# Performance work log

Hardware: AMD Instinct MI355X
Metric: run time of the kernel (lower is better)

The kernel has to match this reference:

```python
import jax, jax.numpy as jnp
import numpy as np

B, N, F_IN, F_OUT = 8, 2048, 128, 128
NEG_BIG = -9e15
LEAKY_SLOPE = 0.01


def setup_inputs() -> dict:
    key = jax.random.key(0)
    k1, k2, k3, k4, k5 = jax.random.split(key, 5)
    features = jax.random.normal(k1, (B, N, F_IN), dtype=jnp.float32)
    adj_matrix = jax.random.randint(k2, (B, N, N), 0, 2, dtype=jnp.int32)
    mask = jnp.ones((B, N), dtype=jnp.float32)
    # linear: W [in,out], b [out]; attention: a [2*out] (no bias)
    W = jax.random.normal(k3, (F_IN, F_OUT), dtype=jnp.float32) / np.sqrt(F_IN)
    b = jnp.zeros((F_OUT,), dtype=jnp.float32)
    a = jax.random.normal(k4, (2 * F_OUT,), dtype=jnp.float32) / np.sqrt(2 * F_OUT)
    return {"features": features, "adj_matrix": adj_matrix, "mask": mask,
            "W": W, "b": b, "a": a}


def reference(features, adj_matrix, mask, W, b, a):
    h = jnp.einsum("bni,io->bno", features, W) + b  # [B,N,F_OUT]
    # attention(concat([h_i, h_j])) == h_i @ a_src + h_j @ a_dst
    a_src, a_dst = a[:F_OUT], a[F_OUT:]
    e = (h @ a_src)[:, :, None] + (h @ a_dst)[:, None, :]  # [B,N,N]
    e = jnp.where(e >= 0, e, LEAKY_SLOPE * e)  # leaky_relu
    scores = jnp.where(adj_matrix > 0, e, jnp.float32(NEG_BIG))
    attention = jax.nn.softmax(scores, axis=-1)
    aggregated = jnp.einsum("bnm,bmo->bno", attention, h)  # [B,N,F_OUT]
    aggregated = aggregated * mask[:, :, None]
    return aggregated
```

## Files before the change

### kernel.cpp

```cpp
#include <hip/hip_runtime.h>

#define BB 8
#define NN 2048
#define FF 128
#define RB 32
#define MT 128

typedef short bh8 __attribute__((ext_vector_type(8)));
typedef float fl4 __attribute__((ext_vector_type(4)));
typedef unsigned short u16;
typedef unsigned long long u64;

__device__ __forceinline__ u16 f2bf(float x) {
    unsigned u = __float_as_uint(x);
    return (u16)((u + 0x7FFFu + ((u >> 16) & 1u)) >> 16);
}

__global__ __launch_bounds__(256) void k_h(
    const float* __restrict__ feat, const float* __restrict__ W,
    const float* __restrict__ bias, const float* __restrict__ a,
    u16* __restrict__ htg, float* __restrict__ esrc, float* __restrict__ edst)
{
    __shared__ float fsh[8][FF];
    __shared__ float red[2][2][8];
    const int t = threadIdx.x;
    const long row0 = (long)blockIdx.x * 8;

    ((float4*)&fsh[0][0])[t] = ((const float4*)(feat + row0 * FF))[t];
    __syncthreads();

    const int o = t & 127;
    const int half = t >> 7;
    float acc[4] = {0.f, 0.f, 0.f, 0.f};
    #pragma unroll 4
    for (int k = 0; k < FF; ++k) {
        const float w = W[k * FF + o];
        #pragma unroll
        for (int r = 0; r < 4; ++r)
            acc[r] = fmaf(fsh[half * 4 + r][k], w, acc[r]);
    }
    const float bo = bias[o];
    const float as = a[o];
    const float ad = a[FF + o];
    float ps[4], pd[4];
    #pragma unroll
    for (int r = 0; r < 4; ++r) {
        acc[r] += bo;
        ps[r] = acc[r] * as;
        pd[r] = acc[r] * ad;
    }
    {
        const int bI = (int)(row0 >> 11);
        const int nloc = (int)(row0 & 2047) + half * 4;
        ushort4 hv;
        hv.x = f2bf(acc[0]); hv.y = f2bf(acc[1]);
        hv.z = f2bf(acc[2]); hv.w = f2bf(acc[3]);
        *(ushort4*)&htg[((long)bI * FF + o) * NN + nloc] = hv;
    }
    #pragma unroll
    for (int r = 0; r < 4; ++r) {
        #pragma unroll
        for (int off = 32; off > 0; off >>= 1) {
            ps[r] += __shfl_down(ps[r], off, 64);
            pd[r] += __shfl_down(pd[r], off, 64);
        }
    }
    const int wv = (t >> 6) & 1;
    if ((t & 63) == 0) {
        #pragma unroll
        for (int r = 0; r < 4; ++r) {
            red[half][wv][r]     = ps[r];
            red[half][wv][4 + r] = pd[r];
        }
    }
    __syncthreads();
    if (t < 16) {
        const int hh = t >> 3, idx = t & 7;
        const float v = red[hh][0][idx] + red[hh][1][idx];
        const long row = row0 + hh * 4 + (idx & 3);
        if (idx < 4) esrc[row] = v;
        else         edst[row] = v;
    }
}

__global__ __launch_bounds__(256) void k_pack(
    const int* __restrict__ adj, u64* __restrict__ bm)
{
    const int t = threadIdx.x;
    const int w = t >> 6, lane = t & 63;
    const long row0 = (long)blockIdx.x * 8;
    #pragma unroll 8
    for (int i = 0; i < 64; ++i) {
        const int row = 2 * w + (i >> 5);
        const int chunk = i & 31;
        const int av = adj[(row0 + row) * NN + chunk * 64 + lane];
        const u64 m64 = __ballot(av > 0);
        if (lane == 0) bm[(row0 + row) * 32 + chunk] = m64;
    }
}

__global__ __launch_bounds__(256, 2) void k_attn(
    const u64* __restrict__ bm, const float* __restrict__ mask,
    const u16* __restrict__ htg, const float* __restrict__ esrc,
    const float* __restrict__ edst, float* __restrict__ out)
{
    __shared__ float accbuf[4][RB][FF + 4];
    __shared__ float psum_sh[4][RB];

    const int t = threadIdx.x;
    const int b = blockIdx.x & 7;
    const int n0 = (blockIdx.x >> 3) * RB;
    const int w = t >> 6, lane = t & 63;
    const int lr = lane & 15, g = lane >> 4;

    float gmx = -3.4e38f;
    {
        const float4* edp = (const float4*)(edst + b * NN);
        #pragma unroll
        for (int i = 0; i < 8; ++i) {
            const float4 v = edp[lane + 64 * i];
            gmx = fmaxf(gmx, fmaxf(fmaxf(v.x, v.y), fmaxf(v.z, v.w)));
        }
        #pragma unroll
        for (int off = 32; off > 0; off >>= 1)
            gmx = fmaxf(gmx, __shfl_xor(gmx, off, 64));
    }

    const float es0 = esrc[b * NN + n0 + lr];
    const float es1 = esrc[b * NN + n0 + 16 + lr];
    const float tA = es0 + gmx; const float M0 = (tA >= 0.f) ? tA : 0.01f * tA;
    const float tB = es1 + gmx; const float M1 = (tB >= 0.f) ? tB : 0.01f * tB;

    const uint4* bmb = (const uint4*)(bm + ((long)b * NN + n0) * 32);
    const float* edb = edst + b * NN;
    const u16* hB = htg + (long)b * FF * NN;

    fl4 acc0[8], acc1[8];
    #pragma unroll
    for (int ct = 0; ct < 8; ++ct) {
        acc0[ct] = (fl4){0.f, 0.f, 0.f, 0.f};
        acc1[ct] = (fl4){0.f, 0.f, 0.f, 0.f};
    }
    float psum0 = 0.f, psum1 = 0.f;

    uint4 bmA0 = bmb[lr * 16 + w];
    uint4 bmA1 = bmb[(16 + lr) * 16 + w];

    #pragma unroll 1
    for (int it = 0; it < 4; ++it) {
        const int m0 = (w + 4 * it) * MT;
        const int base = m0 + g * 8;

        float4 ed[8];
        #pragma unroll
        for (int kc = 0; kc < 4; ++kc) {
            ed[2 * kc]     = *(const float4*)(edb + base + kc * 32);
            ed[2 * kc + 1] = *(const float4*)(edb + base + kc * 32 + 4);
        }
        bh8 bfA[8];
        #pragma unroll
        for (int ct = 0; ct < 8; ++ct)
            bfA[ct] = *(const bh8*)(hB + (long)(ct * 16 + lr) * NN + base);
        const int itn = (it + 1) & 3;
        uint4 bmB0 = bmb[lr * 16 + w + 4 * itn];
        uint4 bmB1 = bmb[(16 + lr) * 16 + w + 4 * itn];

        bh8 af0[4], af1[4];
        #pragma unroll
        for (int kc = 0; kc < 4; ++kc) {
            const unsigned w0 = (kc == 0) ? bmA0.x : (kc == 1) ? bmA0.y
                              : (kc == 2) ? bmA0.z : bmA0.w;
            const unsigned w1 = (kc == 0) ? bmA1.x : (kc == 1) ? bmA1.y
                              : (kc == 2) ? bmA1.z : bmA1.w;
            const unsigned by0 = (w0 >> (8 * g)) & 0xFFu;
            const unsigned by1 = (w1 >> (8 * g)) & 0xFFu;
            const float4 e0 = ed[2 * kc], e1 = ed[2 * kc + 1];
            const float ee[8] = {e0.x, e0.y, e0.z, e0.w, e1.x, e1.y, e1.z, e1.w};
            u16 p0[8], p1[8];
            #pragma unroll
            for (int j = 0; j < 8; ++j) {
                float x0 = es0 + ee[j]; x0 = (x0 >= 0.f) ? x0 : 0.01f * x0;
                float x1 = es1 + ee[j]; x1 = (x1 >= 0.f) ? x1 : 0.01f * x1;
                const float v0 = ((by0 >> j) & 1u) ? __expf(x0 - M0) : 0.f;
                const float v1 = ((by1 >> j) & 1u) ? __expf(x1 - M1) : 0.f;
                const u16 u0 = f2bf(v0), u1 = f2bf(v1);
                p0[j] = u0; p1[j] = u1;
                psum0 += __uint_as_float((unsigned)u0 << 16);
                psum1 += __uint_as_float((unsigned)u1 << 16);
            }
            af0[kc] = (bh8){(short)p0[0], (short)p0[1], (short)p0[2], (short)p0[3],
                            (short)p0[4], (short)p0[5], (short)p0[6], (short)p0[7]};
            af1[kc] = (bh8){(short)p1[0], (short)p1[1], (short)p1[2], (short)p1[3],
                            (short)p1[4], (short)p1[5], (short)p1[6], (short)p1[7]};
        }

        #pragma unroll
        for (int kc = 0; kc < 4; ++kc) {
            bh8 bfB[8];
            if (kc < 3) {
                #pragma unroll
                for (int ct = 0; ct < 8; ++ct)
                    bfB[ct] = *(const bh8*)(hB + (long)(ct * 16 + lr) * NN
                                            + base + (kc + 1) * 32);
            }
            #pragma unroll
            for (int ct = 0; ct < 8; ++ct) {
                acc0[ct] = __builtin_amdgcn_mfma_f32_16x16x32_bf16(af0[kc], bfA[ct], acc0[ct], 0, 0, 0);
                acc1[ct] = __builtin_amdgcn_mfma_f32_16x16x32_bf16(af1[kc], bfA[ct], acc1[ct], 0, 0, 0);
            }
            if (kc < 3) {
                #pragma unroll
                for (int ct = 0; ct < 8; ++ct) bfA[ct] = bfB[ct];
            }
        }
        bmA0 = bmB0; bmA1 = bmB1;
    }

    psum0 += __shfl_xor(psum0, 16, 64);
    psum0 += __shfl_xor(psum0, 32, 64);
    psum1 += __shfl_xor(psum1, 16, 64);
    psum1 += __shfl_xor(psum1, 32, 64);
    if (lane < 16) {
        psum_sh[w][lr] = psum0;
        psum_sh[w][16 + lr] = psum1;
    }

    #pragma unroll
    for (int ct = 0; ct < 8; ++ct)
        #pragma unroll
        for (int reg = 0; reg < 4; ++reg) {
            accbuf[w][g * 4 + reg][ct * 16 + lr]      = acc0[ct][reg];
            accbuf[w][16 + g * 4 + reg][ct * 16 + lr] = acc1[ct][reg];
        }
    __syncthreads();

    #pragma unroll
    for (int rep = 0; rep < 4; ++rep) {
        const int idx = t + 256 * rep;
        const int r = idx >> 5;
        const int c4 = (idx & 31) * 4;
        const float4 s0 = *(const float4*)&accbuf[0][r][c4];
        const float4 s1 = *(const float4*)&accbuf[1][r][c4];
        const float4 s2 = *(const float4*)&accbuf[2][r][c4];
        const float4 s3 = *(const float4*)&accbuf[3][r][c4];
        const float ps = psum_sh[0][r] + psum_sh[1][r] + psum_sh[2][r] + psum_sh[3][r];
        const float sc = mask[b * NN + n0 + r] / ps;
        float4 o;
        o.x = (s0.x + s1.x + s2.x + s3.x) * sc;
        o.y = (s0.y + s1.y + s2.y + s3.y) * sc;
        o.z = (s0.z + s1.z + s2.z + s3.z) * sc;
        o.w = (s0.w + s1.w + s2.w + s3.w) * sc;
        *(float4*)&out[((long)b * NN + n0 + r) * FF + c4] = o;
    }
}

extern "C" void kernel_launch(void* const* d_in, const int* in_sizes, int n_in,
                              void* d_out, int out_size, void* d_ws, size_t ws_size,
                              hipStream_t stream)
{
    const float* feat = (const float*)d_in[0];
    const int*   adj  = (const int*)d_in[1];
    const float* mask = (const float*)d_in[2];
    const float* W    = (const float*)d_in[3];
    const float* bias = (const float*)d_in[4];
    const float* a    = (const float*)d_in[5];
    float* out = (float*)d_out;

    u16*   htg  = (u16*)d_ws;
    float* esrc = (float*)(htg + (size_t)BB * FF * NN);
    float* edst = esrc + BB * NN;
    u64*   bmp  = (u64*)(edst + BB * NN);

    k_pack<<<BB * NN / 8, 256, 0, stream>>>(adj, bmp);
    k_h   <<<BB * NN / 8, 256, 0, stream>>>(feat, W, bias, a, htg, esrc, edst);
    k_attn<<<BB * (NN / RB), 256, 0, stream>>>(bmp, mask, htg, esrc, edst, out);
}
```

Measured before the change: 86.15 us.

## Fuse pack into projection kernel, factor exp, precompute global max, pipeline B loads

Merges the adjacency bit-packing into the projection kernel, which now also computes the per-batch max of edst with an atomicMax on order-preserving bit patterns. The projection kernel additionally stores exp(edst) and exp(0.01*edst). The attention kernel replaces its per-element exp with a multiply by per-row factors, choosing the branch by comparing against exp(-esrc). The attention loop is fully unrolled with a triple-buffered B-operand prefetch and sched barriers. The final reduction is done in registers through a smaller shared buffer, which removes one exp per score and the redundant max scan at the cost of an extra memset and more register pressure.

```diff
diff --git a/kernel.cpp b/kernel.cpp
--- a/kernel.cpp
+++ b/kernel.cpp
@@ -1,4 +1,5 @@
 #include <hip/hip_runtime.h>
+#include <hip/hip_bf16.h>
 
 #define BB 8
 #define NN 2048
@@ -10,16 +11,34 @@
 typedef float fl4 __attribute__((ext_vector_type(4)));
 typedef unsigned short u16;
 typedef unsigned long long u64;
+typedef union { bh8 v; unsigned u[4]; } bh8u;
 
 __device__ __forceinline__ u16 f2bf(float x) {
     unsigned u = __float_as_uint(x);
     return (u16)((u + 0x7FFFu + ((u >> 16) & 1u)) >> 16);
 }
 
-__global__ __launch_bounds__(256) void k_h(
-    const float* __restrict__ feat, const float* __restrict__ W,
-    const float* __restrict__ bias, const float* __restrict__ a,
-    u16* __restrict__ htg, float* __restrict__ esrc, float* __restrict__ edst)
+__device__ __forceinline__ void loadB(bh8 (&buf)[8], const u16* hB, int lr, int kbase) {
+    #pragma unroll
+    for (int ct = 0; ct < 8; ++ct)
+        buf[ct] = *(const bh8*)(hB + (ct * 16 + lr) * NN + kbase);
+}
+
+__device__ __forceinline__ void mfma16(bh8 a0, bh8 a1, const bh8 (&buf)[8],
+                                       fl4 (&c0)[8], fl4 (&c1)[8]) {
+    #pragma unroll
+    for (int ct = 0; ct < 8; ++ct) {
+        c0[ct] = __builtin_amdgcn_mfma_f32_16x16x32_bf16(a0, buf[ct], c0[ct], 0, 0, 0);
+        c1[ct] = __builtin_amdgcn_mfma_f32_16x16x32_bf16(a1, buf[ct], c1[ct], 0, 0, 0);
+    }
+}
+
+__global__ __launch_bounds__(256) void k_hp(
+    const float* __restrict__ feat, const int* __restrict__ adj,
+    const float* __restrict__ W, const float* __restrict__ bias,
+    const float* __restrict__ a, u16* __restrict__ htg,
+    float* __restrict__ esrc, float* __restrict__ eed, float* __restrict__ eed2,
+    unsigned* __restrict__ gmaxu, u64* __restrict__ bm)
 {
     __shared__ float fsh[8][FF];
     __shared__ float red[2][2][8];
@@ -78,33 +97,43 @@
         const int hh = t >> 3, idx = t & 7;
         const float v = red[hh][0][idx] + red[hh][1][idx];
         const long row = row0 + hh * 4 + (idx & 3);
-        if (idx < 4) esrc[row] = v;
-        else         edst[row] = v;
-    }
-}
-
-__global__ __launch_bounds__(256) void k_pack(
-    const int* __restrict__ adj, u64* __restrict__ bm)
-{
-    const int t = threadIdx.x;
-    const int w = t >> 6, lane = t & 63;
-    const long row0 = (long)blockIdx.x * 8;
-    #pragma unroll 8
-    for (int i = 0; i < 64; ++i) {
-        const int row = 2 * w + (i >> 5);
-        const int chunk = i & 31;
-        const int av = adj[(row0 + row) * NN + chunk * 64 + lane];
-        const u64 m64 = __ballot(av > 0);
-        if (lane == 0) bm[(row0 + row) * 32 + chunk] = m64;
+        if (idx < 4) {
+            esrc[row] = v;
+        } else {
+            eed[row]  = __expf(v);
+            eed2[row] = __expf(0.01f * v);
+        }
+        float mv = (idx >= 4) ? v : -3.4e38f;
+        #pragma unroll
+        for (int off = 8; off > 0; off >>= 1)
+            mv = fmaxf(mv, __shfl_xor(mv, off, 16));
+        if (t == 0) {
+            unsigned bu = __float_as_uint(mv);
+            bu = (bu & 0x80000000u) ? ~bu : (bu | 0x80000000u);
+            atomicMax(gmaxu + (int)(row0 >> 11), bu);
+        }
+    }
+
+    {
+        const int w2 = t >> 6, lane = t & 63;
+        #pragma unroll 8
+        for (int i = 0; i < 64; ++i) {
+            const int row = 2 * w2 + (i >> 5);
+            const int chunk = i & 31;
+            const int av = adj[(row0 + row) * NN + chunk * 64 + lane];
+            const u64 m64 = __ballot(av > 0);
+            if (lane == 0) bm[(row0 + row) * 32 + chunk] = m64;
+        }
     }
 }
 
 __global__ __launch_bounds__(256, 2) void k_attn(
     const u64* __restrict__ bm, const float* __restrict__ mask,
     const u16* __restrict__ htg, const float* __restrict__ esrc,
-    const float* __restrict__ edst, float* __restrict__ out)
+    const float* __restrict__ eed, const float* __restrict__ eed2,
+    const unsigned* __restrict__ gmaxu, float* __restrict__ out)
 {
-    __shared__ float accbuf[4][RB][FF + 4];
+    __shared__ float accbuf[2][RB][FF + 4];
     __shared__ float psum_sh[4][RB];
 
     const int t = threadIdx.x;
@@ -113,26 +142,18 @@
     const int w = t >> 6, lane = t & 63;
     const int lr = lane & 15, g = lane >> 4;
 
-    float gmx = -3.4e38f;
-    {
-        const float4* edp = (const float4*)(edst + b * NN);
-        #pragma unroll
-        for (int i = 0; i < 8; ++i) {
-            const float4 v = edp[lane + 64 * i];
-            gmx = fmaxf(gmx, fmaxf(fmaxf(v.x, v.y), fmaxf(v.z, v.w)));
-        }
-        #pragma unroll
-        for (int off = 32; off > 0; off >>= 1)
-            gmx = fmaxf(gmx, __shfl_xor(gmx, off, 64));
-    }
-
+    const unsigned gu = gmaxu[b];
+    const float gm = __uint_as_float((gu & 0x80000000u) ? (gu & 0x7FFFFFFFu) : ~gu);
     const float es0 = esrc[b * NN + n0 + lr];
     const float es1 = esrc[b * NN + n0 + 16 + lr];
-    const float tA = es0 + gmx; const float M0 = (tA >= 0.f) ? tA : 0.01f * tA;
-    const float tB = es1 + gmx; const float M1 = (tB >= 0.f) ? tB : 0.01f * tB;
+    const float m0t = es0 + gm; const float M0 = fmaxf(m0t, 0.01f * m0t);
+    const float m1t = es1 + gm; const float M1 = fmaxf(m1t, 0.01f * m1t);
+    const float A0 = __expf(es0 - M0), Bv0 = __expf(0.01f * es0 - M0), T0 = __expf(-es0);
+    const float A1 = __expf(es1 - M1), Bv1 = __expf(0.01f * es1 - M1), T1 = __expf(-es1);
 
     const uint4* bmb = (const uint4*)(bm + ((long)b * NN + n0) * 32);
-    const float* edb = edst + b * NN;
+    const float* eeb  = eed  + b * NN;
+    const float* ee2b = eed2 + b * NN;
     const u16* hB = htg + (long)b * FF * NN;
 
     fl4 acc0[8], acc1[8];
@@ -143,77 +164,73 @@
     }
     float psum0 = 0.f, psum1 = 0.f;
 
-    uint4 bmA0 = bmb[lr * 16 + w];
-    uint4 bmA1 = bmb[(16 + lr) * 16 + w];
-
-    #pragma unroll 1
+    bh8 bf0[8], bf1[8], bf2[8];
+    loadB(bf0, hB, lr, w * MT + g * 8);
+    loadB(bf1, hB, lr, w * MT + g * 8 + 32);
+    loadB(bf2, hB, lr, w * MT + g * 8 + 64);
+
+    #pragma unroll
     for (int it = 0; it < 4; ++it) {
-        const int m0 = (w + 4 * it) * MT;
-        const int base = m0 + g * 8;
-
-        float4 ed[8];
+        const int kb = (w + 4 * it) * MT + g * 8;
+        const uint4 bq0 = bmb[lr * 16 + (w + 4 * it)];
+        const uint4 bq1 = bmb[(16 + lr) * 16 + (w + 4 * it)];
+
+        bh8 af0[4], af1[4];
+        float pst0 = 0.f, pst1 = 0.f;
         #pragma unroll
         for (int kc = 0; kc < 4; ++kc) {
-            ed[2 * kc]     = *(const float4*)(edb + base + kc * 32);
-            ed[2 * kc + 1] = *(const float4*)(edb + base + kc * 32 + 4);
-        }
-        bh8 bfA[8];
-        #pragma unroll
-        for (int ct = 0; ct < 8; ++ct)
-            bfA[ct] = *(const bh8*)(hB + (long)(ct * 16 + lr) * NN + base);
-        const int itn = (it + 1) & 3;
-        uint4 bmB0 = bmb[lr * 16 + w + 4 * itn];
-        uint4 bmB1 = bmb[(16 + lr) * 16 + w + 4 * itn];
-
-        bh8 af0[4], af1[4];
+            const unsigned q0 = (kc == 0) ? bq0.x : (kc == 1) ? bq0.y : (kc == 2) ? bq0.z : bq0.w;
+            const unsigned q1 = (kc == 0) ? bq1.x : (kc == 1) ? bq1.y : (kc == 2) ? bq1.z : bq1.w;
+            const unsigned by0 = (q0 >> (8 * g)) & 0xFFu;
+            const unsigned by1 = (q1 >> (8 * g)) & 0xFFu;
+            const float4 Ea = *(const float4*)(eeb + kb + kc * 32);
+            const float4 Eb = *(const float4*)(eeb + kb + kc * 32 + 4);
+            const float4 Fa = *(const float4*)(ee2b + kb + kc * 32);
+            const float4 Fb = *(const float4*)(ee2b + kb + kc * 32 + 4);
+            const float pe[8] = {Ea.x, Ea.y, Ea.z, Ea.w, Eb.x, Eb.y, Eb.z, Eb.w};
+            const float pf[8] = {Fa.x, Fa.y, Fa.z, Fa.w, Fb.x, Fb.y, Fb.z, Fb.w};
+            bh8u pa, pb;
+            float s00 = 0.f, s01 = 0.f, s10 = 0.f, s11 = 0.f;
+            #pragma unroll
+            for (int jj = 0; jj < 4; ++jj) {
+                const int j0 = 2 * jj, j1 = 2 * jj + 1;
+                const float v00 = ((by0 >> j0) & 1u) ? ((pe[j0] >= T0) ? A0 * pe[j0] : Bv0 * pf[j0]) : 0.f;
+                const float v01 = ((by0 >> j1) & 1u) ? ((pe[j1] >= T0) ? A0 * pe[j1] : Bv0 * pf[j1]) : 0.f;
+                const float v10 = ((by1 >> j0) & 1u) ? ((pe[j0] >= T1) ? A1 * pe[j0] : Bv1 * pf[j0]) : 0.f;
+                const float v11 = ((by1 >> j1) & 1u) ? ((pe[j1] >= T1) ? A1 * pe[j1] : Bv1 * pf[j1]) : 0.f;
+                float2 c0f; c0f.x = v00; c0f.y = v01;
+                float2 c1f; c1f.x = v10; c1f.y = v11;
+                __hip_bfloat162 r0 = __float22bfloat162_rn(c0f);
+                __hip_bfloat162 r1 = __float22bfloat162_rn(c1f);
+                const unsigned u0 = *reinterpret_cast<unsigned*>(&r0);
+                const unsigned u1 = *reinterpret_cast<unsigned*>(&r1);
+                pa.u[jj] = u0;
+                pb.u[jj] = u1;
+                s00 += __uint_as_float(u0 << 16);
+                s01 += __uint_as_float(u0 & 0xFFFF0000u);
+                s10 += __uint_as_float(u1 << 16);
+                s11 += __uint_as_float(u1 & 0xFFFF0000u);
+            }
+            pst0 += s00 + s01;
+            pst1 += s10 + s11;
+            af0[kc] = pa.v;
+            af1[kc] = pb.v;
+        }
+        psum0 += pst0;
+        psum1 += pst1;
+        __builtin_amdgcn_sched_barrier(0);
+
         #pragma unroll
         for (int kc = 0; kc < 4; ++kc) {
-            const unsigned w0 = (kc == 0) ? bmA0.x : (kc == 1) ? bmA0.y
-                              : (kc == 2) ? bmA0.z : bmA0.w;
-            const unsigned w1 = (kc == 0) ? bmA1.x : (kc == 1) ? bmA1.y
-                              : (kc == 2) ? bmA1.z : bmA1.w;
-            const unsigned by0 = (w0 >> (8 * g)) & 0xFFu;
-            const unsigned by1 = (w1 >> (8 * g)) & 0xFFu;
-            const float4 e0 = ed[2 * kc], e1 = ed[2 * kc + 1];
-            const float ee[8] = {e0.x, e0.y, e0.z, e0.w, e1.x, e1.y, e1.z, e1.w};
-            u16 p0[8], p1[8];
-            #pragma unroll
-            for (int j = 0; j < 8; ++j) {
-                float x0 = es0 + ee[j]; x0 = (x0 >= 0.f) ? x0 : 0.01f * x0;
-                float x1 = es1 + ee[j]; x1 = (x1 >= 0.f) ? x1 : 0.01f * x1;
-                const float v0 = ((by0 >> j) & 1u) ? __expf(x0 - M0) : 0.f;
-                const float v1 = ((by1 >> j) & 1u) ? __expf(x1 - M1) : 0.f;
-                const u16 u0 = f2bf(v0), u1 = f2bf(v1);
-                p0[j] = u0; p1[j] = u1;
-                psum0 += __uint_as_float((unsigned)u0 << 16);
-                psum1 += __uint_as_float((unsigned)u1 << 16);
-            }
-            af0[kc] = (bh8){(short)p0[0], (short)p0[1], (short)p0[2], (short)p0[3],
-                            (short)p0[4], (short)p0[5], (short)p0[6], (short)p0[7]};
-            af1[kc] = (bh8){(short)p1[0], (short)p1[1], (short)p1[2], (short)p1[3],
-                            (short)p1[4], (short)p1[5], (short)p1[6], (short)p1[7]};
-        }
-
-        #pragma unroll
-        for (int kc = 0; kc < 4; ++kc) {
-            bh8 bfB[8];
-            if (kc < 3) {
-                #pragma unroll
-                for (int ct = 0; ct < 8; ++ct)
-                    bfB[ct] = *(const bh8*)(hB + (long)(ct * 16 + lr) * NN
-                                            + base + (kc + 1) * 32);
-            }
-            #pragma unroll
-            for (int ct = 0; ct < 8; ++ct) {
-                acc0[ct] = __builtin_amdgcn_mfma_f32_16x16x32_bf16(af0[kc], bfA[ct], acc0[ct], 0, 0, 0);
-                acc1[ct] = __builtin_amdgcn_mfma_f32_16x16x32_bf16(af1[kc], bfA[ct], acc1[ct], 0, 0, 0);
-            }
-            if (kc < 3) {
-                #pragma unroll
-                for (int ct = 0; ct < 8; ++ct) bfA[ct] = bfB[ct];
-            }
-        }
-        bmA0 = bmB0; bmA1 = bmB1;
+            const int c = it * 4 + kc;
+            bh8 (&cur)[8] = (c % 3 == 0) ? bf0 : ((c % 3 == 1) ? bf1 : bf2);
+            mfma16(af0[kc], af1[kc], cur, acc0, acc1);
+            if (c + 3 < 16) {
+                const int cn = c + 3;
+                loadB(cur, hB, lr, (w + 4 * (cn >> 2)) * MT + g * 8 + (cn & 3) * 32);
+            }
+            __builtin_amdgcn_sched_barrier(0);
+        }
     }
 
     psum0 += __shfl_xor(psum0, 16, 64);
@@ -225,32 +242,53 @@
         psum_sh[w][16 + lr] = psum1;
     }
 
-    #pragma unroll
-    for (int ct = 0; ct < 8; ++ct)
+    if (w >= 2) {
+        #pragma unroll
+        for (int ct = 0; ct < 8; ++ct)
+            #pragma unroll
+            for (int reg = 0; reg < 4; ++reg) {
+                accbuf[w - 2][g * 4 + reg][ct * 16 + lr]      = acc0[ct][reg];
+                accbuf[w - 2][16 + g * 4 + reg][ct * 16 + lr] = acc1[ct][reg];
+            }
+    }
+    __syncthreads();
+    if (w < 2) {
+        #pragma unroll
+        for (int ct = 0; ct < 8; ++ct)
+            #pragma unroll
+            for (int reg = 0; reg < 4; ++reg) {
+                acc0[ct][reg] += accbuf[w][g * 4 + reg][ct * 16 + lr];
+                acc1[ct][reg] += accbuf[w][16 + g * 4 + reg][ct * 16 + lr];
+            }
+        if (w == 1) {
+            #pragma unroll
+            for (int ct = 0; ct < 8; ++ct)
+                #pragma unroll
+                for (int reg = 0; reg < 4; ++reg) {
+                    accbuf[1][g * 4 + reg][ct * 16 + lr]      = acc0[ct][reg];
+                    accbuf[1][16 + g * 4 + reg][ct * 16 + lr] = acc1[ct][reg];
+                }
+        }
+    }
+    __syncthreads();
+    if (w == 0) {
+        const long obase = ((long)b * NN + n0) * FF;
         #pragma unroll
         for (int reg = 0; reg < 4; ++reg) {
-            accbuf[w][g * 4 + reg][ct * 16 + lr]      = acc0[ct][reg];
-            accbuf[w][16 + g * 4 + reg][ct * 16 + lr] = acc1[ct][reg];
-        }
-    __syncthreads();
-
-    #pragma unroll
-    for (int rep = 0; rep < 4; ++rep) {
-        const int idx = t + 256 * rep;
-        const int r = idx >> 5;
-        const int c4 = (idx & 31) * 4;
-        const float4 s0 = *(const float4*)&accbuf[0][r][c4];
-        const float4 s1 = *(const float4*)&accbuf[1][r][c4];
-        const float4 s2 = *(const float4*)&accbuf[2][r][c4];
-        const float4 s3 = *(const float4*)&accbuf[3][r][c4];
-        const float ps = psum_sh[0][r] + psum_sh[1][r] + psum_sh[2][r] + psum_sh[3][r];
-        const float sc = mask[b * NN + n0 + r] / ps;
-        float4 o;
-        o.x = (s0.x + s1.x + s2.x + s3.x) * sc;
-        o.y = (s0.y + s1.y + s2.y + s3.y) * sc;
-        o.z = (s0.z + s1.z + s2.z + s3.z) * sc;
-        o.w = (s0.w + s1.w + s2.w + s3.w) * sc;
-        *(float4*)&out[((long)b * NN + n0 + r) * FF + c4] = o;
+            const int r0 = g * 4 + reg;
+            const int r1 = 16 + r0;
+            const float pt0 = psum_sh[0][r0] + psum_sh[1][r0] + psum_sh[2][r0] + psum_sh[3][r0];
+            const float pt1 = psum_sh[0][r1] + psum_sh[1][r1] + psum_sh[2][r1] + psum_sh[3][r1];
+            const float sc0 = mask[b * NN + n0 + r0] / pt0;
+            const float sc1 = mask[b * NN + n0 + r1] / pt1;
+            #pragma unroll
+            for (int ct = 0; ct < 8; ++ct) {
+                out[obase + (long)r0 * FF + ct * 16 + lr] =
+                    (acc0[ct][reg] + accbuf[1][r0][ct * 16 + lr]) * sc0;
+                out[obase + (long)r1 * FF + ct * 16 + lr] =
+                    (acc1[ct][reg] + accbuf[1][r1][ct * 16 + lr]) * sc1;
+            }
+        }
     }
 }
 
@@ -266,12 +304,14 @@
     const float* a    = (const float*)d_in[5];
     float* out = (float*)d_out;
 
-    u16*   htg  = (u16*)d_ws;
-    float* esrc = (float*)(htg + (size_t)BB * FF * NN);
-    float* edst = esrc + BB * NN;
-    u64*   bmp  = (u64*)(edst + BB * NN);
-
-    k_pack<<<BB * NN / 8, 256, 0, stream>>>(adj, bmp);
-    k_h   <<<BB * NN / 8, 256, 0, stream>>>(feat, W, bias, a, htg, esrc, edst);
-    k_attn<<<BB * (NN / RB), 256, 0, stream>>>(bmp, mask, htg, esrc, edst, out);
-}
+    u16*      htg   = (u16*)d_ws;
+    float*    esrc  = (float*)(htg + (size_t)BB * FF * NN);
+    float*    eed   = esrc + BB * NN;
+    float*    eed2  = eed + BB * NN;
+    unsigned* gmaxu = (unsigned*)(eed2 + BB * NN);
+    u64*      bmp   = (u64*)(gmaxu + 8);
+
+    hipMemsetAsync(gmaxu, 0, BB * sizeof(unsigned), stream);
+    k_hp  <<<BB * NN / 8, 256, 0, stream>>>(feat, adj, W, bias, a, htg, esrc, eed, eed2, gmaxu, bmp);
+    k_attn<<<BB * (NN / RB), 256, 0, stream>>>(bmp, mask, htg, esrc, eed, eed2, gmaxu, out);
+}
```

Result: slower. 174.9 us (+103.1%).
